# Optimization experiments

Hardware: AMD Instinct MI355X
Metric: run time of the kernel (lower is better)

## Reference

```python
import jax, jax.numpy as jnp
import numpy as np

B, Q, K, D, H = 2, 2048, 2048, 1024, 16
HD = D // H  # 64
EPS = 1e-6  # flax LayerNorm default epsilon


def setup_inputs() -> dict:
    key = jax.random.key(0)
    ks = jax.random.split(key, 12)
    s = 1.0 / np.sqrt(D)  # lecun_normal-like scale
    inputs_q = jax.random.normal(ks[0], (B, Q, D), jnp.float32)
    bias = jax.random.normal(ks[1], (B, 1, Q, K), jnp.float32)
    mask = jax.random.randint(ks[2], (B, 1, Q, K), 0, 2).astype(jnp.bool_)
    wq = jax.random.normal(ks[3], (D, H, HD), jnp.float32) * s
    wk = jax.random.normal(ks[4], (D, H, HD), jnp.float32) * s
    wv = jax.random.normal(ks[5], (D, H, HD), jnp.float32) * s
    bq = jnp.zeros((H, HD), jnp.float32)
    bk = jnp.zeros((H, HD), jnp.float32)
    bv = jnp.zeros((H, HD), jnp.float32)
    q_scale = jnp.ones((HD,), jnp.float32)
    k_scale = jnp.ones((HD,), jnp.float32)
    wo = jax.random.normal(ks[6], (H, HD, D), jnp.float32) * s
    bo = jnp.zeros((D,), jnp.float32)
    return dict(inputs_q=inputs_q, bias=bias, mask=mask, wq=wq, bq=bq,
                wk=wk, bk=bk, wv=wv, bv=bv, q_scale=q_scale, k_scale=k_scale,
                wo=wo, bo=bo)


def _layernorm_nobias(x, scale):
    # normalize over last axis (head_dim), no bias, like flax LayerNorm(use_bias=False)
    mean = jnp.mean(x, axis=-1, keepdims=True)
    var = jnp.mean(jnp.square(x - mean), axis=-1, keepdims=True)
    return (x - mean) * jax.lax.rsqrt(var + EPS) * scale


def reference(inputs_q, bias, mask, wq, bq, wk, bk, wv, bv, q_scale, k_scale, wo, bo):
    # QKV projections (self-attention: k and v inputs default to inputs_q)
    q = jnp.einsum('bqd,dhe->bqhe', inputs_q, wq) + bq  # [B,Q,H,HD]
    k = jnp.einsum('bkd,dhe->bkhe', inputs_q, wk) + bk  # [B,K,H,HD]
    v = jnp.einsum('bkd,dhe->bkhe', inputs_q, wv) + bv  # [B,K,H,HD]
    # optional QK layernorm (normalize_qk=True)
    q = _layernorm_nobias(q, q_scale)
    k = _layernorm_nobias(k, k_scale)
    # attention weights
    q = q / jnp.sqrt(jnp.asarray(q.shape[-1], q.dtype))
    attn = jnp.einsum('bqhe,bkhe->bhqk', q, k)  # [B,H,Q,K]
    attn = attn + bias
    big_neg = jnp.finfo(q.dtype).min
    attn = jnp.where(mask, attn, big_neg)
    attn = jax.nn.softmax(attn.astype(jnp.float32), axis=-1).astype(q.dtype)
    # weighted values + output projection
    x = jnp.einsum('bhqk,bkhe->bqhe', attn, v)  # [B,Q,H,HD]
    out = jnp.einsum('bqhe,heo->bqo', x, wo) + bo  # [B,Q,D]
    return out
```

## Files before the change

### kernel.cpp

```cpp
#include <hip/hip_runtime.h>
#include <cstdint>
#include <cstddef>

typedef __bf16 bf16_t;
typedef __bf16 bf16x8 __attribute__((ext_vector_type(8)));
typedef __bf16 bf16x4 __attribute__((ext_vector_type(4)));
typedef _Float16 f16_t;
typedef _Float16 f16x4 __attribute__((ext_vector_type(4)));
typedef float f32x4 __attribute__((ext_vector_type(4)));

constexpr int BB = 2, SS = 2048, DD = 1024, HH = 16, HDIM = 64;
constexpr int BS = BB * SS;
constexpr float LOG2E = 1.4426950408889634f;

__device__ __forceinline__ void glds16(const void* g, void* l) {
  __builtin_amdgcn_global_load_lds((const __attribute__((address_space(1))) void*)g,
                                   (__attribute__((address_space(3))) void*)l, 16, 0, 0);
}

__global__ __launch_bounds__(256) void prep_fused(
    const float* __restrict__ x, const float* __restrict__ wq, const float* __restrict__ wk,
    const float* __restrict__ wv, const float* __restrict__ wo, const float* __restrict__ bias,
    const int* __restrict__ mask, bf16_t* __restrict__ xb, bf16_t* __restrict__ wqkv_t,
    bf16_t* __restrict__ wo_t, f16_t* __restrict__ vmq) {
  __shared__ __align__(16) char smem[18432];
  float (*tile)[65] = (float(*)[65])smem;
  f16_t (*btile)[72] = (f16_t(*)[72])smem;
  int bid = blockIdx.x;
  int t = threadIdx.x;
  if (bid < 4096) {
    int i = bid * 256 + t;
    float4 v = ((const float4*)x)[i];
    union { bf16_t h[4]; uint2 u; } o;
    o.h[0] = (bf16_t)v.x; o.h[1] = (bf16_t)v.y; o.h[2] = (bf16_t)v.z; o.h[3] = (bf16_t)v.w;
    ((uint2*)xb)[i] = o.u;
  } else if (bid < 5120) {
    int id = bid - 4096;
    int which = id >> 8, tr = (id >> 4) & 15, tc = id & 15;
    const float* src = (which == 0) ? wq : (which == 1) ? wk : (which == 2) ? wv : wo;
    bf16_t* dst = (which < 3) ? wqkv_t : wo_t;
    int noff = (which < 3) ? which * 1024 : 0;
#pragma unroll
    for (int p = 0; p < 4; ++p) {
      int e = (p * 256 + t) * 4;
      int r = e >> 6, c = e & 63;
      float4 v = *(const float4*)&src[(size_t)(tr * 64 + r) * 1024 + tc * 64 + c];
      tile[r][c] = v.x; tile[r][c + 1] = v.y; tile[r][c + 2] = v.z; tile[r][c + 3] = v.w;
    }
    __syncthreads();
#pragma unroll
    for (int p = 0; p < 4; ++p) {
      int e = (p * 256 + t) * 4;
      int r = e >> 6, c = e & 63;
      union { bf16_t h[4]; uint2 u; } o;
#pragma unroll
      for (int j = 0; j < 4; ++j) o.h[j] = (bf16_t)tile[c + j][r];
      *(uint2*)&dst[(size_t)(noff + tc * 64 + r) * 1024 + tr * 64 + c] = o.u;
    }
  } else {
    int id = bid - 5120;
    int b = id >> 9, qt = (id >> 5) & 15, kt = id & 31;
    size_t base_in = ((size_t)(b * 2048 + qt * 128)) * 2048 + kt * 64;
#pragma unroll
    for (int p = 0; p < 4; ++p) {
      int c = p * 256 + t;
      int qr = c >> 3, k8 = (c & 7) * 8;
      const float* bp = &bias[base_in + (size_t)qr * 2048 + k8];
      const int* mp = &mask[base_in + (size_t)qr * 2048 + k8];
      float4 b0 = *(const float4*)bp;
      float4 b1 = *(const float4*)(bp + 4);
      int4 m0 = *(const int4*)mp;
      int4 m1 = *(const int4*)(mp + 4);
      union { f16_t h[8]; uint4 u; } o;
      o.h[0] = m0.x ? (f16_t)__builtin_amdgcn_exp2f(b0.x * LOG2E - 8.0f) : (f16_t)0.0f;
      o.h[1] = m0.y ? (f16_t)__builtin_amdgcn_exp2f(b0.y * LOG2E - 8.0f) : (f16_t)0.0f;
      o.h[2] = m0.z ? (f16_t)__builtin_amdgcn_exp2f(b0.z * LOG2E - 8.0f) : (f16_t)0.0f;
      o.h[3] = m0.w ? (f16_t)__builtin_amdgcn_exp2f(b0.w * LOG2E - 8.0f) : (f16_t)0.0f;
      o.h[4] = m1.x ? (f16_t)__builtin_amdgcn_exp2f(b1.x * LOG2E - 8.0f) : (f16_t)0.0f;
      o.h[5] = m1.y ? (f16_t)__builtin_amdgcn_exp2f(b1.y * LOG2E - 8.0f) : (f16_t)0.0f;
      o.h[6] = m1.z ? (f16_t)__builtin_amdgcn_exp2f(b1.z * LOG2E - 8.0f) : (f16_t)0.0f;
      o.h[7] = m1.w ? (f16_t)__builtin_amdgcn_exp2f(b1.w * LOG2E - 8.0f) : (f16_t)0.0f;
      *(uint4*)&btile[qr][k8] = o.u;
    }
    __syncthreads();
    int w = t >> 6, lane = t & 63, lo = lane & 15, quad = lane >> 4;
    size_t obase = ((size_t)(((b * 16 + qt) * 32 + kt) * 16)) * 64;
#pragma unroll
    for (int j = 0; j < 4; ++j) {
      int row = w * 32 + (j >> 1) * 16 + lo;
      int mbl = 2 * (j & 1);
      union { f16_t h[8]; uint4 u; } o;
#pragma unroll
      for (int e = 0; e < 8; ++e)
        o.h[e] = btile[row][(mbl + (e >> 2)) * 16 + quad * 4 + (e & 3)];
      ((uint4*)vmq)[obase + (w * 4 + j) * 64 + lane] = o.u;
    }
  }
}

template <bool OUT_F32, int BNT>
__global__ __launch_bounds__(256) void gemm_bt(const bf16_t* __restrict__ A,
                                               const bf16_t* __restrict__ Bt,
                                               bf16_t* __restrict__ Cb, float* __restrict__ Cf,
                                               const float* __restrict__ bias, int M, int N,
                                               int Kd) {
  constexpr int WNW = BNT / 2;
  constexpr int NFR = WNW / 16;
  __shared__ __align__(16) bf16_t As[128][32];
  __shared__ __align__(16) bf16_t Bs[BNT][32];
  int tid = threadIdx.x;
  int lane = tid & 63, w = tid >> 6;
  int lo = lane & 15, quad = lane >> 4;
  int wm = w >> 1, wn = w & 1;
  int nbx = gridDim.x;
  int nwg = nbx * gridDim.y;
  int lid = blockIdx.y * nbx + blockIdx.x;
  int sid = (lid & 7) * (nwg >> 3) + (lid >> 3);
  int m0 = (sid / nbx) * 128, n0 = (sid % nbx) * BNT;
  int srow = lane >> 2;
  int scol = (lane & 3) * 8;
  f32x4 acc[4][NFR] = {};
  for (int kk = 0; kk < Kd; kk += 32) {
#pragma unroll
    for (int t = 0; t < 2; ++t) {
      int rb = (w * 2 + t) * 16;
      glds16(&A[(size_t)(m0 + rb + srow) * Kd + kk + scol], &As[rb][0]);
      if (rb < BNT) glds16(&Bt[(size_t)(n0 + rb + srow) * Kd + kk + scol], &Bs[rb][0]);
    }
    asm volatile("s_waitcnt vmcnt(0)" ::: "memory");
    __syncthreads();
    bf16x8 am[4], bn[NFR];
#pragma unroll
    for (int i = 0; i < 4; ++i) am[i] = *(const bf16x8*)&As[wm * 64 + i * 16 + lo][quad * 8];
#pragma unroll
    for (int i = 0; i < NFR; ++i) bn[i] = *(const bf16x8*)&Bs[wn * WNW + i * 16 + lo][quad * 8];
#pragma unroll
    for (int mi = 0; mi < 4; ++mi)
#pragma unroll
      for (int ni = 0; ni < NFR; ++ni)
        acc[mi][ni] = __builtin_amdgcn_mfma_f32_16x16x32_bf16(am[mi], bn[ni], acc[mi][ni], 0, 0, 0);
    __syncthreads();
  }
#pragma unroll
  for (int mi = 0; mi < 4; ++mi) {
#pragma unroll
    for (int ni = 0; ni < NFR; ++ni) {
#pragma unroll
      for (int r = 0; r < 4; ++r) {
        int row = m0 + wm * 64 + mi * 16 + quad * 4 + r;
        int col = n0 + wn * WNW + ni * 16 + lo;
        float v = acc[mi][ni][r];
        if (OUT_F32)
          Cf[(size_t)row * N + col] = v + bias[col];
        else
          Cb[(size_t)row * N + col] = (bf16_t)v;
      }
    }
  }
}

__global__ __launch_bounds__(256) void postqkv(const bf16_t* __restrict__ Cqkv,
                                               const float* __restrict__ bq,
                                               const float* __restrict__ bk,
                                               const float* __restrict__ bv,
                                               const float* __restrict__ q_scale,
                                               const float* __restrict__ k_scale,
                                               bf16_t* __restrict__ qb, bf16_t* __restrict__ kb,
                                               f16_t* __restrict__ vt) {
  __shared__ float tile[64][65];
  int bid = blockIdx.x;
  int t = threadIdx.x;
  if (bid < 4096) {
    int vec2 = bid * 32 + ((t >> 6) << 3) + ((t & 63) >> 3);
    int mode = vec2 >> 16;
    int vec = vec2 & 65535;
    int bs = vec >> 4, h = vec & 15;
    int b = bs >> 11, s = bs & 2047;
    int e0 = (t & 7) * 8;
    const float* badd = (mode == 0) ? bq : bk;
    const float* sc = (mode == 0) ? q_scale : k_scale;
    bf16_t* dst = (mode == 0) ? qb : kb;
    bf16x8 v8 = *(const bf16x8*)&Cqkv[(size_t)bs * 3072 + mode * 1024 + h * 64 + e0];
    float xv[8];
    float sum = 0.0f;
#pragma unroll
    for (int j = 0; j < 8; ++j) { xv[j] = (float)v8[j] + badd[h * 64 + e0 + j]; sum += xv[j]; }
#pragma unroll
    for (int off = 1; off <= 4; off <<= 1) sum += __shfl_xor(sum, off, 64);
    float mean = sum * (1.0f / 64.0f);
    float vs = 0.0f;
#pragma unroll
    for (int j = 0; j < 8; ++j) { xv[j] -= mean; vs += xv[j] * xv[j]; }
#pragma unroll
    for (int off = 1; off <= 4; off <<= 1) vs += __shfl_xor(vs, off, 64);
    float rstd = rsqrtf(vs * (1.0f / 64.0f) + 1e-6f);
    if (mode == 0) rstd *= 0.125f * LOG2E;
    union { bf16_t h[8]; uint4 u; } o;
#pragma unroll
    for (int j = 0; j < 8; ++j) o.h[j] = (bf16_t)(xv[j] * rstd * sc[e0 + j]);
    int ch = (mode == 0) ? (t & 7) : ((t & 7) ^ (s & 7));
    *(uint4*)&dst[(size_t)((b * 16 + h) * 2048 + s) * 64 + ch * 8] = o.u;
  } else {
    int id2 = bid - 4096;
    int st = id2 & 31, h = (id2 >> 5) & 15, b = id2 >> 9;
#pragma unroll
    for (int p = 0; p < 2; ++p) {
      int e = (p * 256 + t) * 8;
      int r = e >> 6, c = e & 63;
      bf16x8 v8 = *(const bf16x8*)&Cqkv[(size_t)(b * SS + st * 64 + r) * 3072 + 2048 + h * 64 + c];
#pragma unroll
      for (int j = 0; j < 8; ++j) tile[r][c + j] = (float)v8[j] + bv[h * 64 + c + j];
    }
    __syncthreads();
#pragma unroll
    for (int p = 0; p < 2; ++p) {
      int e = (p * 256 + t) * 8;
      int r = e >> 6, c = e & 63;
      union { f16_t h[8]; uint4 u; } o;
#pragma unroll
      for (int j = 0; j < 8; ++j) o.h[j] = (f16_t)tile[c + j][r];
      *(uint4*)&vt[(size_t)((b * HH + h) * HDIM + r) * SS + st * 64 +
                   ((((c >> 3) ^ (r & 7)) << 3))] = o.u;
    }
  }
}

#define ATTN_TILE(KT, CUR, STG, VMC)                                                          \
  {                                                                                           \
    if ((KT) == 31) { asm volatile("s_waitcnt vmcnt(0)" ::: "memory"); }                      \
    else            { asm volatile("s_waitcnt vmcnt(8)" ::: "memory"); }                      \
    __builtin_amdgcn_s_barrier();                                                             \
    if ((KT) + 2 < 32) {                                                                      \
      int k0n = ((KT) + 2) * 64;                                                              \
      _Pragma("unroll") for (int tt = 0; tt < 2; ++tt) {                                      \
        int i = w * 2 + tt;                                                                   \
        int r = i * 8 + (lane >> 3);                                                          \
        glds16(&kbase[(size_t)(k0n + r) * 64 + ((lane & 7) << 3)], (STG) + i * 1024);         \
        glds16(&vbase[(size_t)r * SS + k0n + ((lane & 7) << 3)], (STG) + 8192 + i * 1024);    \
      }                                                                                       \
    }                                                                                         \
    __builtin_amdgcn_s_setprio(1);                                                            \
    bf16x8 ka[4][2];                                                                          \
    _Pragma("unroll") for (int mb = 0; mb < 4; ++mb)                                          \
      _Pragma("unroll") for (int ec = 0; ec < 2; ++ec)                                        \
        ka[mb][ec] = *(const bf16x8*)((CUR) + (mb * 16 + lo) * 128 +                          \
                                      ((((ec << 2) | quad) ^ (lo & 7)) << 4));                \
    f16x4 pf[2][4];                                                                           \
    _Pragma("unroll") for (int qg = 0; qg < 2; ++qg)                                          \
      _Pragma("unroll") for (int mb = 0; mb < 4; ++mb) {                                      \
        f32x4 s = {};                                                                         \
        s = __builtin_amdgcn_mfma_f32_16x16x32_bf16(ka[mb][0], bqf[qg][0], s, 0, 0, 0);       \
        s = __builtin_amdgcn_mfma_f32_16x16x32_bf16(ka[mb][1], bqf[qg][1], s, 0, 0, 0);       \
        f16x4 p4;                                                                             \
        p4[0] = (f16_t)__builtin_amdgcn_exp2f(s[0]);                                          \
        p4[1] = (f16_t)__builtin_amdgcn_exp2f(s[1]);                                          \
        p4[2] = (f16_t)__builtin_amdgcn_exp2f(s[2]);                                          \
        p4[3] = (f16_t)__builtin_amdgcn_exp2f(s[3]);                                          \
        pf[qg][mb] = p4 * VMC[qg * 2 + (mb >> 1)].q[mb & 1];                                  \
      }                                                                                       \
    __builtin_amdgcn_s_setprio(0);                                                            \
    if ((KT) + 2 < 32) {           \
      _Pragma("unroll") for (int j = 0; j < 4; ++j)                                           \
        VMC[j].u = vmtile[(size_t)((KT) + 2) * 1024 + j * 64];                                \
    }                                                                                         \
    __builtin_amdgcn_s_setprio(1);                                                            \
    _Pragma("unroll") for (int mb = 0; mb < 4; ++mb) {                                        \
      _Pragma("unroll") for (int eb = 0; eb < 4; ++eb) {                                      \
        f16x4 va = *(const f16x4*)((CUR) + 8192 + (eb * 16 + lo) * 128 +                      \
                                   (((((mb << 1) | (quad >> 1)) ^ (lo & 7)) << 4) |           \
                                    ((quad & 1) << 3)));                                      \
        _Pragma("unroll") for (int qg = 0; qg < 2; ++qg)                                      \
          ot[qg][eb] =                                                                        \
              __builtin_amdgcn_mfma_f32_16x16x16f16(va, pf[qg][mb], ot[qg][eb], 0, 0, 0);     \
      }                                                                                       \
      _Pragma("unroll") for (int qg = 0; qg < 2; ++qg)                                        \
        lacc[qg] = __builtin_amdgcn_mfma_f32_16x16x16f16(ones, pf[qg][mb], lacc[qg], 0, 0, 0);\
    }                                                                                         \
    __builtin_amdgcn_s_setprio(0);                                                            \
  }

__global__ __launch_bounds__(256, 2) void attn_kernel(const bf16_t* __restrict__ qb,
                                                      const bf16_t* __restrict__ kb,
                                                      const f16_t* __restrict__ vt,
                                                      const f16_t* __restrict__ vmq,
                                                      bf16_t* __restrict__ xout) {
  __shared__ __align__(16) char lds[4][16384];
  int tid = threadIdx.x;
  int lane = tid & 63, w = tid >> 6;
  int lo = lane & 15, quad = lane >> 4;
  int lid = blockIdx.x;
  int sid = ((lid & 7) << 6) | (lid >> 3);
  int qt = sid & 15, h = (sid >> 4) & 15, b = sid >> 8;
  size_t headoff = (size_t)(b * HH + h) * SS * HDIM;
  int q0 = qt * 128 + w * 32;
  const bf16_t* kbase = kb + headoff;
  const f16_t* vbase = vt + headoff;
  const uint4* vmtile =
      (const uint4*)vmq + ((size_t)((b * 16 + qt) * 32) * 16 + w * 4) * 64 + lane;

  bf16x8 bqf[2][2];
#pragma unroll
  for (int qg = 0; qg < 2; ++qg)
#pragma unroll
    for (int ec = 0; ec < 2; ++ec)
      bqf[qg][ec] =
          *(const bf16x8*)&qb[headoff + (size_t)(q0 + qg * 16 + lo) * HDIM + ec * 32 + quad * 8];

  f16x4 ones;
#pragma unroll
  for (int j = 0; j < 4; ++j) ones[j] = (f16_t)1.0f;

  f32x4 ot[2][4] = {};
  f32x4 lacc[2] = {};

  union VM { uint4 u; f16x4 q[2]; };
  VM vma[4], vmb[4];

#pragma unroll
  for (int tt = 0; tt < 2; ++tt) {
    int i = w * 2 + tt;
    int r = i * 8 + (lane >> 3);
    glds16(&kbase[(size_t)r * 64 + ((lane & 7) << 3)], lds[0] + i * 1024);
    glds16(&vbase[(size_t)r * SS + ((lane & 7) << 3)], lds[0] + 8192 + i * 1024);
  }
#pragma unroll
  for (int j = 0; j < 4; ++j) vma[j].u = vmtile[j * 64];
#pragma unroll
  for (int tt = 0; tt < 2; ++tt) {
    int i = w * 2 + tt;
    int r = i * 8 + (lane >> 3);
    glds16(&kbase[(size_t)(64 + r) * 64 + ((lane & 7) << 3)], lds[1] + i * 1024);
    glds16(&vbase[(size_t)r * SS + 64 + ((lane & 7) << 3)], lds[1] + 8192 + i * 1024);
  }
#pragma unroll
  for (int j = 0; j < 4; ++j) vmb[j].u = vmtile[1024 + j * 64];

#pragma unroll 1
  for (int kt0 = 0; kt0 < 32; kt0 += 4) {
    ATTN_TILE(kt0 + 0, lds[0], lds[2], vma)
    ATTN_TILE(kt0 + 1, lds[1], lds[3], vmb)
    ATTN_TILE(kt0 + 2, lds[2], lds[0], vma)
    ATTN_TILE(kt0 + 3, lds[3], lds[1], vmb)
  }

#pragma unroll
  for (int qg = 0; qg < 2; ++qg) {
    float rl = 1.0f / lacc[qg][0];
    int q = q0 + qg * 16 + lo;
#pragma unroll
    for (int eb = 0; eb < 4; ++eb) {
      union { bf16_t h4[4]; uint2 u; } o;
#pragma unroll
      for (int r = 0; r < 4; ++r) o.h4[r] = (bf16_t)(ot[qg][eb][r] * rl);
      *(uint2*)&xout[(size_t)(b * SS + q) * DD + h * 64 + eb * 16 + quad * 4] = o.u;
    }
  }
}

extern "C" void kernel_launch(void* const* d_in, const int* in_sizes, int n_in, void* d_out,
                              int out_size, void* d_ws, size_t ws_size, hipStream_t stream) {
  const float* inputs_q = (const float*)d_in[0];
  const float* bias = (const float*)d_in[1];
  const int* mask = (const int*)d_in[2];
  const float* wq = (const float*)d_in[3];
  const float* bq = (const float*)d_in[4];
  const float* wk = (const float*)d_in[5];
  const float* bk = (const float*)d_in[6];
  const float* wv = (const float*)d_in[7];
  const float* bv = (const float*)d_in[8];
  const float* q_scale = (const float*)d_in[9];
  const float* k_scale = (const float*)d_in[10];
  const float* wo = (const float*)d_in[11];
  const float* bo = (const float*)d_in[12];
  float* out = (float*)d_out;

  char* ws = (char*)d_ws;
  bf16_t* wo_t   = (bf16_t*)(ws);
  f16_t*  vmq    = (f16_t*)(ws + ((size_t)2 << 20));
  bf16_t* cqkv   = (bf16_t*)(ws + ((size_t)19 << 20));
  bf16_t* xattn  = (bf16_t*)(ws + ((size_t)19 << 20));
  bf16_t* xb     = (bf16_t*)(ws + ((size_t)43 << 20));
  bf16_t* qb2    = (bf16_t*)(ws + ((size_t)43 << 20));
  bf16_t* wqkv_t = (bf16_t*)(ws + ((size_t)51 << 20));
  bf16_t* kb2    = (bf16_t*)(ws + ((size_t)51 << 20));
  f16_t*  vtb    = (f16_t*)(ws + ((size_t)59 << 20));

  prep_fused<<<6144, 256, 0, stream>>>(inputs_q, wq, wk, wv, wo, bias, mask, xb, wqkv_t, wo_t, vmq);
  gemm_bt<false, 128><<<dim3(24, 32), 256, 0, stream>>>(xb, wqkv_t, cqkv, nullptr, nullptr, BS,
                                                        3072, DD);
  postqkv<<<5120, 256, 0, stream>>>(cqkv, bq, bk, bv, q_scale, k_scale, qb2, kb2, vtb);
  attn_kernel<<<512, 256, 0, stream>>>(qb2, kb2, vtb, vmq, xattn);
  gemm_bt<true, 64><<<dim3(16, 32), 256, 0, stream>>>(xattn, wo_t, nullptr, out, bo, BS, 1024, DD);
}
```

Baseline: 271.4 us.

## Triple-buffer GEMM LDS staging and fuse Q/K layernorm into QKV GEMM epilogue

Replaces the single-buffered GEMM main loop with a three-stage LDS ring. The next-next tile is issued before the MFMAs and only a partial vmcnt wait is done, so global loads overlap compute and one barrier per iteration is removed. The QKV GEMM epilogue now applies bias and layernorm to the Q and K columns and writes head-major (swizzled for K) outputs directly, leaving a smaller kernel that only transposes V. The trade-offs are higher LDS use per block, scalar strided bf16 stores in the epilogue, and new workspace regions for Q and K.

```diff
diff --git a/kernel.cpp b/kernel.cpp
--- a/kernel.cpp
+++ b/kernel.cpp
@@ -17,6 +17,8 @@
   __builtin_amdgcn_global_load_lds((const __attribute__((address_space(1))) void*)g,
                                    (__attribute__((address_space(3))) void*)l, 16, 0, 0);
 }
+
+#define MEMFENCE asm volatile("" ::: "memory")
 
 __global__ __launch_bounds__(256) void prep_fused(
     const float* __restrict__ x, const float* __restrict__ wq, const float* __restrict__ wk,
@@ -98,16 +100,17 @@
   }
 }
 
-template <bool OUT_F32, int BNT>
-__global__ __launch_bounds__(256) void gemm_bt(const bf16_t* __restrict__ A,
-                                               const bf16_t* __restrict__ Bt,
-                                               bf16_t* __restrict__ Cb, float* __restrict__ Cf,
-                                               const float* __restrict__ bias, int M, int N,
-                                               int Kd) {
+template <int EPI, int BNT>
+__global__ __launch_bounds__(256) void gemm_bt(
+    const bf16_t* __restrict__ A, const bf16_t* __restrict__ Bt, bf16_t* __restrict__ Cb,
+    float* __restrict__ Cf, const float* __restrict__ bias, int M, int N, int Kd,
+    bf16_t* __restrict__ qb, bf16_t* __restrict__ kb, const float* __restrict__ bq,
+    const float* __restrict__ bk, const float* __restrict__ q_scale,
+    const float* __restrict__ k_scale) {
   constexpr int WNW = BNT / 2;
   constexpr int NFR = WNW / 16;
-  __shared__ __align__(16) bf16_t As[128][32];
-  __shared__ __align__(16) bf16_t Bs[BNT][32];
+  __shared__ __align__(16) bf16_t As[3][128][32];
+  __shared__ __align__(16) bf16_t Bs[3][BNT][32];
   int tid = threadIdx.x;
   int lane = tid & 63, w = tid >> 6;
   int lo = lane & 15, quad = lane >> 4;
@@ -119,109 +122,144 @@
   int m0 = (sid / nbx) * 128, n0 = (sid % nbx) * BNT;
   int srow = lane >> 2;
   int scol = (lane & 3) * 8;
+  const int NK = Kd >> 5;
   f32x4 acc[4][NFR] = {};
-  for (int kk = 0; kk < Kd; kk += 32) {
-#pragma unroll
-    for (int t = 0; t < 2; ++t) {
-      int rb = (w * 2 + t) * 16;
-      glds16(&A[(size_t)(m0 + rb + srow) * Kd + kk + scol], &As[rb][0]);
-      if (rb < BNT) glds16(&Bt[(size_t)(n0 + rb + srow) * Kd + kk + scol], &Bs[rb][0]);
-    }
-    asm volatile("s_waitcnt vmcnt(0)" ::: "memory");
-    __syncthreads();
+
+  auto stage = [&](int kk, int buf) {
+    int r0 = (w * 2) * 16, r1 = (w * 2 + 1) * 16;
+    glds16(&A[(size_t)(m0 + r0 + srow) * Kd + kk * 32 + scol], &As[buf][r0][0]);
+    glds16(&A[(size_t)(m0 + r1 + srow) * Kd + kk * 32 + scol], &As[buf][r1][0]);
+    if constexpr (BNT == 128) {
+      glds16(&Bt[(size_t)(n0 + r0 + srow) * Kd + kk * 32 + scol], &Bs[buf][r0][0]);
+      glds16(&Bt[(size_t)(n0 + r1 + srow) * Kd + kk * 32 + scol], &Bs[buf][r1][0]);
+    } else {
+      int rb = w * 16;
+      glds16(&Bt[(size_t)(n0 + rb + srow) * Kd + kk * 32 + scol], &Bs[buf][rb][0]);
+    }
+  };
+
+  stage(0, 0);
+  MEMFENCE;
+  stage(1, 1);
+  int b0 = 0, b2 = 2;
+#pragma unroll 1
+  for (int kk = 0; kk < NK; ++kk) {
+    if (kk == NK - 1) {
+      asm volatile("s_waitcnt vmcnt(0)" ::: "memory");
+    } else if constexpr (BNT == 128) {
+      asm volatile("s_waitcnt vmcnt(4)" ::: "memory");
+    } else {
+      asm volatile("s_waitcnt vmcnt(3)" ::: "memory");
+    }
+    __builtin_amdgcn_s_barrier();
+    MEMFENCE;
+    if (kk + 2 < NK) stage(kk + 2, b2);
+    __builtin_amdgcn_s_setprio(1);
     bf16x8 am[4], bn[NFR];
 #pragma unroll
-    for (int i = 0; i < 4; ++i) am[i] = *(const bf16x8*)&As[wm * 64 + i * 16 + lo][quad * 8];
-#pragma unroll
-    for (int i = 0; i < NFR; ++i) bn[i] = *(const bf16x8*)&Bs[wn * WNW + i * 16 + lo][quad * 8];
+    for (int i = 0; i < 4; ++i)
+      am[i] = *(const bf16x8*)&As[b0][wm * 64 + i * 16 + lo][quad * 8];
+#pragma unroll
+    for (int i = 0; i < NFR; ++i)
+      bn[i] = *(const bf16x8*)&Bs[b0][wn * WNW + i * 16 + lo][quad * 8];
 #pragma unroll
     for (int mi = 0; mi < 4; ++mi)
 #pragma unroll
       for (int ni = 0; ni < NFR; ++ni)
         acc[mi][ni] = __builtin_amdgcn_mfma_f32_16x16x32_bf16(am[mi], bn[ni], acc[mi][ni], 0, 0, 0);
-    __syncthreads();
-  }
-#pragma unroll
-  for (int mi = 0; mi < 4; ++mi) {
-#pragma unroll
-    for (int ni = 0; ni < NFR; ++ni) {
-#pragma unroll
-      for (int r = 0; r < 4; ++r) {
-        int row = m0 + wm * 64 + mi * 16 + quad * 4 + r;
-        int col = n0 + wn * WNW + ni * 16 + lo;
-        float v = acc[mi][ni][r];
-        if (OUT_F32)
-          Cf[(size_t)row * N + col] = v + bias[col];
-        else
-          Cb[(size_t)row * N + col] = (bf16_t)v;
+    __builtin_amdgcn_s_setprio(0);
+    b0 = (b0 == 2) ? 0 : b0 + 1;
+    b2 = (b2 == 2) ? 0 : b2 + 1;
+  }
+
+  bool plain = true;
+  if constexpr (EPI == 2) {
+    int which = n0 >> 10;
+    if (which < 2) {
+      plain = false;
+      const float* badd = (which == 0) ? bq : bk;
+      const float* sc = (which == 0) ? q_scale : k_scale;
+      int hcol = (n0 + wn * WNW) & 1023;
+      int hh = hcol >> 6;
+#pragma unroll
+      for (int mi = 0; mi < 4; ++mi) {
+#pragma unroll
+        for (int r = 0; r < 4; ++r) {
+          int row = m0 + wm * 64 + mi * 16 + quad * 4 + r;
+          float xv[NFR];
+          float sm = 0.0f;
+#pragma unroll
+          for (int ni = 0; ni < NFR; ++ni) {
+            xv[ni] = acc[mi][ni][r] + badd[hcol + ni * 16 + lo];
+            sm += xv[ni];
+          }
+#pragma unroll
+          for (int off = 1; off <= 8; off <<= 1) sm += __shfl_xor(sm, off, 64);
+          float mean = sm * (1.0f / 64.0f);
+          float vs = 0.0f;
+#pragma unroll
+          for (int ni = 0; ni < NFR; ++ni) { xv[ni] -= mean; vs += xv[ni] * xv[ni]; }
+#pragma unroll
+          for (int off = 1; off <= 8; off <<= 1) vs += __shfl_xor(vs, off, 64);
+          float rstd = rsqrtf(vs * (1.0f / 64.0f) + 1e-6f);
+          if (which == 0) rstd *= 0.125f * LOG2E;
+          int b = row >> 11, s = row & 2047;
+          bf16_t* dst = ((which == 0) ? qb : kb) + (size_t)((b * 16 + hh) * 2048 + s) * 64;
+#pragma unroll
+          for (int ni = 0; ni < NFR; ++ni) {
+            int e = ni * 16 + lo;
+            int eo = (which == 0) ? e : ((((e >> 3) ^ (s & 7)) << 3) | (e & 7));
+            dst[eo] = (bf16_t)(xv[ni] * rstd * sc[e]);
+          }
+        }
       }
     }
   }
-}
-
-__global__ __launch_bounds__(256) void postqkv(const bf16_t* __restrict__ Cqkv,
-                                               const float* __restrict__ bq,
-                                               const float* __restrict__ bk,
-                                               const float* __restrict__ bv,
-                                               const float* __restrict__ q_scale,
-                                               const float* __restrict__ k_scale,
-                                               bf16_t* __restrict__ qb, bf16_t* __restrict__ kb,
-                                               f16_t* __restrict__ vt) {
+  if (plain) {
+#pragma unroll
+    for (int mi = 0; mi < 4; ++mi) {
+#pragma unroll
+      for (int ni = 0; ni < NFR; ++ni) {
+#pragma unroll
+        for (int r = 0; r < 4; ++r) {
+          int row = m0 + wm * 64 + mi * 16 + quad * 4 + r;
+          int col = n0 + wn * WNW + ni * 16 + lo;
+          float v = acc[mi][ni][r];
+          if (EPI == 1)
+            Cf[(size_t)row * N + col] = v + bias[col];
+          else
+            Cb[(size_t)row * N + col] = (bf16_t)v;
+        }
+      }
+    }
+  }
+}
+
+__global__ __launch_bounds__(256) void postv(const bf16_t* __restrict__ Cqkv,
+                                             const float* __restrict__ bv,
+                                             f16_t* __restrict__ vt) {
   __shared__ float tile[64][65];
-  int bid = blockIdx.x;
+  int id2 = blockIdx.x;
   int t = threadIdx.x;
-  if (bid < 4096) {
-    int vec2 = bid * 32 + ((t >> 6) << 3) + ((t & 63) >> 3);
-    int mode = vec2 >> 16;
-    int vec = vec2 & 65535;
-    int bs = vec >> 4, h = vec & 15;
-    int b = bs >> 11, s = bs & 2047;
-    int e0 = (t & 7) * 8;
-    const float* badd = (mode == 0) ? bq : bk;
-    const float* sc = (mode == 0) ? q_scale : k_scale;
-    bf16_t* dst = (mode == 0) ? qb : kb;
-    bf16x8 v8 = *(const bf16x8*)&Cqkv[(size_t)bs * 3072 + mode * 1024 + h * 64 + e0];
-    float xv[8];
-    float sum = 0.0f;
-#pragma unroll
-    for (int j = 0; j < 8; ++j) { xv[j] = (float)v8[j] + badd[h * 64 + e0 + j]; sum += xv[j]; }
-#pragma unroll
-    for (int off = 1; off <= 4; off <<= 1) sum += __shfl_xor(sum, off, 64);
-    float mean = sum * (1.0f / 64.0f);
-    float vs = 0.0f;
-#pragma unroll
-    for (int j = 0; j < 8; ++j) { xv[j] -= mean; vs += xv[j] * xv[j]; }
-#pragma unroll
-    for (int off = 1; off <= 4; off <<= 1) vs += __shfl_xor(vs, off, 64);
-    float rstd = rsqrtf(vs * (1.0f / 64.0f) + 1e-6f);
-    if (mode == 0) rstd *= 0.125f * LOG2E;
-    union { bf16_t h[8]; uint4 u; } o;
-#pragma unroll
-    for (int j = 0; j < 8; ++j) o.h[j] = (bf16_t)(xv[j] * rstd * sc[e0 + j]);
-    int ch = (mode == 0) ? (t & 7) : ((t & 7) ^ (s & 7));
-    *(uint4*)&dst[(size_t)((b * 16 + h) * 2048 + s) * 64 + ch * 8] = o.u;
-  } else {
-    int id2 = bid - 4096;
-    int st = id2 & 31, h = (id2 >> 5) & 15, b = id2 >> 9;
-#pragma unroll
-    for (int p = 0; p < 2; ++p) {
-      int e = (p * 256 + t) * 8;
-      int r = e >> 6, c = e & 63;
-      bf16x8 v8 = *(const bf16x8*)&Cqkv[(size_t)(b * SS + st * 64 + r) * 3072 + 2048 + h * 64 + c];
-#pragma unroll
-      for (int j = 0; j < 8; ++j) tile[r][c + j] = (float)v8[j] + bv[h * 64 + c + j];
-    }
-    __syncthreads();
-#pragma unroll
-    for (int p = 0; p < 2; ++p) {
-      int e = (p * 256 + t) * 8;
-      int r = e >> 6, c = e & 63;
-      union { f16_t h[8]; uint4 u; } o;
-#pragma unroll
-      for (int j = 0; j < 8; ++j) o.h[j] = (f16_t)tile[c + j][r];
-      *(uint4*)&vt[(size_t)((b * HH + h) * HDIM + r) * SS + st * 64 +
-                   ((((c >> 3) ^ (r & 7)) << 3))] = o.u;
-    }
+  int st = id2 & 31, h = (id2 >> 5) & 15, b = id2 >> 9;
+#pragma unroll
+  for (int p = 0; p < 2; ++p) {
+    int e = (p * 256 + t) * 8;
+    int r = e >> 6, c = e & 63;
+    bf16x8 v8 = *(const bf16x8*)&Cqkv[(size_t)(b * SS + st * 64 + r) * 3072 + 2048 + h * 64 + c];
+#pragma unroll
+    for (int j = 0; j < 8; ++j) tile[r][c + j] = (float)v8[j] + bv[h * 64 + c + j];
+  }
+  __syncthreads();
+#pragma unroll
+  for (int p = 0; p < 2; ++p) {
+    int e = (p * 256 + t) * 8;
+    int r = e >> 6, c = e & 63;
+    union { f16_t h[8]; uint4 u; } o;
+#pragma unroll
+    for (int j = 0; j < 8; ++j) o.h[j] = (f16_t)tile[c + j][r];
+    *(uint4*)&vt[(size_t)((b * HH + h) * HDIM + r) * SS + st * 64 +
+                 ((((c >> 3) ^ (r & 7)) << 3))] = o.u;
   }
 }
 
@@ -323,8 +361,10 @@
     glds16(&kbase[(size_t)r * 64 + ((lane & 7) << 3)], lds[0] + i * 1024);
     glds16(&vbase[(size_t)r * SS + ((lane & 7) << 3)], lds[0] + 8192 + i * 1024);
   }
+  MEMFENCE;
 #pragma unroll
   for (int j = 0; j < 4; ++j) vma[j].u = vmtile[j * 64];
+  MEMFENCE;
 #pragma unroll
   for (int tt = 0; tt < 2; ++tt) {
     int i = w * 2 + tt;
@@ -332,6 +372,7 @@
     glds16(&kbase[(size_t)(64 + r) * 64 + ((lane & 7) << 3)], lds[1] + i * 1024);
     glds16(&vbase[(size_t)r * SS + 64 + ((lane & 7) << 3)], lds[1] + 8192 + i * 1024);
   }
+  MEMFENCE;
 #pragma unroll
   for (int j = 0; j < 4; ++j) vmb[j].u = vmtile[1024 + j * 64];
 
@@ -380,15 +421,17 @@
   bf16_t* cqkv   = (bf16_t*)(ws + ((size_t)19 << 20));
   bf16_t* xattn  = (bf16_t*)(ws + ((size_t)19 << 20));
   bf16_t* xb     = (bf16_t*)(ws + ((size_t)43 << 20));
-  bf16_t* qb2    = (bf16_t*)(ws + ((size_t)43 << 20));
   bf16_t* wqkv_t = (bf16_t*)(ws + ((size_t)51 << 20));
-  bf16_t* kb2    = (bf16_t*)(ws + ((size_t)51 << 20));
   f16_t*  vtb    = (f16_t*)(ws + ((size_t)59 << 20));
+  bf16_t* qb2    = (bf16_t*)(ws + ((size_t)67 << 20));
+  bf16_t* kb2    = (bf16_t*)(ws + ((size_t)75 << 20));
 
   prep_fused<<<6144, 256, 0, stream>>>(inputs_q, wq, wk, wv, wo, bias, mask, xb, wqkv_t, wo_t, vmq);
-  gemm_bt<false, 128><<<dim3(24, 32), 256, 0, stream>>>(xb, wqkv_t, cqkv, nullptr, nullptr, BS,
-                                                        3072, DD);
-  postqkv<<<5120, 256, 0, stream>>>(cqkv, bq, bk, bv, q_scale, k_scale, qb2, kb2, vtb);
+  gemm_bt<2, 128><<<dim3(24, 32), 256, 0, stream>>>(xb, wqkv_t, cqkv, nullptr, nullptr, BS, 3072,
+                                                    DD, qb2, kb2, bq, bk, q_scale, k_scale);
+  postv<<<1024, 256, 0, stream>>>(cqkv, bv, vtb);
   attn_kernel<<<512, 256, 0, stream>>>(qb2, kb2, vtb, vmq, xattn);
-  gemm_bt<true, 64><<<dim3(16, 32), 256, 0, stream>>>(xattn, wo_t, nullptr, out, bo, BS, 1024, DD);
-}
+  gemm_bt<1, 64><<<dim3(16, 32), 256, 0, stream>>>(xattn, wo_t, nullptr, out, bo, BS, 1024, DD,
+                                                   nullptr, nullptr, nullptr, nullptr, nullptr,
+                                                   nullptr);
+}
```

New measurement: 286.7 us. 1.06x slower.
